# Kernel tuning notes

Hardware: AMD Instinct MI355X
Metric: run time of the kernel (lower is better)

The kernel has to match this reference:

```python
import jax, jax.numpy as jnp
import numpy as np

D = 512      # n_embd
H = 8        # n_head
L = 2        # n_layer (per stack)
T = 2048     # sequence length / block_size
B = 1        # batch
BANDS = (999, 9)  # band_width for [phase, tool] stacks
EPS = 1e-5


def _sinusoidal(n_pos, dim):
    pos = np.arange(n_pos)[:, None].astype(np.float64)
    j = np.arange(dim)[None, :]
    angle = pos / np.power(10000.0, 2 * (j // 2) / dim)
    out = np.zeros((n_pos, dim), np.float32)
    out[:, 0::2] = np.sin(angle[:, 0::2])
    out[:, 1::2] = np.cos(angle[:, 1::2])
    return jnp.asarray(out)


def setup_inputs() -> dict:
    key = jax.random.key(0)
    ks = jax.random.split(key, 8)
    s = 0.02
    rn = lambda k, shp: jax.random.normal(k, shp, jnp.float32) * s
    inp = {
        "x": jax.random.normal(ks[0], (B, T, D), jnp.float32),
        "pos_emb": _sinusoidal(T, D),            # sinusoidal, frozen
        # leading dim 2 = [phase stack, tool stack], then layer dim L
        "ln1_w": jnp.ones((2, L, D)), "ln1_b": jnp.zeros((2, L, D)),
        "ln2_w": jnp.ones((2, L, D)), "ln2_b": jnp.zeros((2, L, D)),
        "Wq": rn(ks[1], (2, L, D, D)), "bq": jnp.zeros((2, L, D)),
        "Wk": rn(ks[2], (2, L, D, D)), "bk": jnp.zeros((2, L, D)),
        "Wv": rn(ks[3], (2, L, D, D)), "bv": jnp.zeros((2, L, D)),
        "Wo": rn(ks[4], (2, L, D, D)), "bo": jnp.zeros((2, L, D)),
        "W1": rn(ks[5], (2, L, D, 2 * D)), "b1": jnp.zeros((2, L, 2 * D)),
        "W2": rn(ks[6], (2, L, 2 * D, D)), "b2": jnp.zeros((2, L, D)),
        "lnf_w": jnp.ones((D,)), "lnf_b": jnp.zeros((D,)),
    }
    return inp


def _ln(x, w, b):
    mu = x.mean(-1, keepdims=True)
    var = ((x - mu) ** 2).mean(-1, keepdims=True)
    return (x - mu) / jnp.sqrt(var + EPS) * w + b


def _attn(x, Wq, bq, Wk, bk, Wv, bv, Wo, bo, bw):
    Bx, Tx, _ = x.shape
    Dh = D // H
    heads = lambda W, b: (x @ W + b).reshape(Bx, Tx, H, Dh).transpose(0, 2, 1, 3)
    q, k, v = heads(Wq, bq), heads(Wk, bk), heads(Wv, bv)
    att = jnp.einsum('bhqd,bhkd->bhqk', q, k) / jnp.sqrt(jnp.float32(Dh))
    i = jnp.arange(Tx)[:, None]
    j = jnp.arange(Tx)[None, :]
    mask = (j <= i) & (j >= i - bw)  # causal band
    att = jnp.where(mask, att, -jnp.inf)
    att = jax.nn.softmax(att, axis=-1)
    y = jnp.einsum('bhqk,bhkd->bhqd', att, v).transpose(0, 2, 1, 3).reshape(Bx, Tx, D)
    return y @ Wo + bo


def reference(x, pos_emb, ln1_w, ln1_b, ln2_w, ln2_b,
              Wq, bq, Wk, bk, Wv, bv, Wo, bo,
              W1, b1, W2, b2, lnf_w, lnf_b):
    Tx = x.shape[1]
    h0 = x + pos_emb[None, :Tx]
    outs = []
    for s in range(2):  # phase stack, tool stack
        bw = BANDS[s]
        h = h0
        for l in range(L):
            h = h + _attn(_ln(h, ln1_w[s, l], ln1_b[s, l]),
                          Wq[s, l], bq[s, l], Wk[s, l], bk[s, l],
                          Wv[s, l], bv[s, l], Wo[s, l], bo[s, l], bw)
            hm = _ln(h, ln2_w[s, l], ln2_b[s, l])
            h = h + (jax.nn.gelu(hm @ W1[s, l] + b1[s, l], approximate=False)
                     @ W2[s, l] + b2[s, l])
        outs.append(_ln(h, lnf_w, lnf_b))
    return (outs[0], outs[1])
```

## Files before the change

### kernel.cpp

```cpp
#include <hip/hip_runtime.h>
#include <stdint.h>

#define T 2048
#define D 512
#define NH 8
#define DH 64
#define L 2

typedef float floatx4 __attribute__((ext_vector_type(4)));
typedef short shortx8 __attribute__((ext_vector_type(8)));
typedef unsigned short u16;
typedef unsigned short u16x4 __attribute__((ext_vector_type(4)));

__device__ __forceinline__ u16 f2bf(float f) {
    union { float f; uint32_t u; } c; c.f = f;
    uint32_t u = c.u;
    u += 0x7fffu + ((u >> 16) & 1u);
    return (u16)(u >> 16);
}

__device__ __forceinline__ float bf2f(u16 v) {
    union { uint32_t u; float f; } c; c.u = ((uint32_t)v) << 16;
    return c.f;
}

__device__ __forceinline__ void load_lds16(const void* g, void* l) {
    __builtin_amdgcn_global_load_lds((const __attribute__((address_space(1))) void*)g,
                                     (__attribute__((address_space(3))) void*)l,
                                     16, 0, 0);
}

struct TransJobs {
    const float* src[6];
    u16* dst[6];
    const float* x;
    const float* pos;
    u16* h;
};

__global__ __launch_bounds__(256) void pre_kernel(TransJobs j) {
    __shared__ float tile[32][33];
    int tid = threadIdx.x;
    if (blockIdx.z == 24) {
        int idx = (blockIdx.y * 32 + blockIdx.x) * 256 + tid;
        float4 xv = ((const float4*)j.x)[idx];
        float4 pv = ((const float4*)j.pos)[idx];
        u16x4 hh;
        hh[0] = f2bf(xv.x + pv.x); hh[1] = f2bf(xv.y + pv.y);
        hh[2] = f2bf(xv.z + pv.z); hh[3] = f2bf(xv.w + pv.w);
        ((u16x4*)j.h)[idx] = hh;
        ((u16x4*)j.h)[idx + (T * D / 4)] = hh;
        return;
    }
    int m = blockIdx.z >> 2, slice = blockIdx.z & 3;
    int R = (m == 5) ? 1024 : 512;
    int C = (m == 4) ? 1024 : 512;
    if (blockIdx.x * 32 >= C || blockIdx.y * 32 >= R) return;
    const float* in = j.src[m] + (size_t)slice * R * C;
    u16* out = j.dst[m] + (size_t)slice * R * C;
    int tx = tid & 31, ty = tid >> 5;
    int x = blockIdx.x * 32 + tx;
    int y0 = blockIdx.y * 32;
#pragma unroll
    for (int i = 0; i < 4; i++)
        tile[ty + i * 8][tx] = in[(size_t)(y0 + ty + i * 8) * C + x];
    __syncthreads();
    int ox = y0 + tx;
#pragma unroll
    for (int i = 0; i < 4; i++)
        out[(size_t)(blockIdx.x * 32 + ty + i * 8) * R + ox] = f2bf(tile[tx][ty + i * 8]);
}

__global__ __launch_bounds__(256) void ln_res_kernel(u16* __restrict__ h,
                                                     const u16* __restrict__ part,
                                                     const float* __restrict__ wp,
                                                     const float* __restrict__ bp,
                                                     u16* __restrict__ out, int l) {
    int row = blockIdx.x * 4 + (threadIdx.x >> 6);
    int lane = threadIdx.x & 63;
    int s = row >> 11;
    int c0 = lane * 4;
    u16* xr = h + (size_t)row * D;
    u16x4 h0 = *(const u16x4*)(xr + c0);
    u16x4 h1 = *(const u16x4*)(xr + c0 + 256);
    float4 v0, v1;
    v0.x = bf2f(h0[0]); v0.y = bf2f(h0[1]); v0.z = bf2f(h0[2]); v0.w = bf2f(h0[3]);
    v1.x = bf2f(h1[0]); v1.y = bf2f(h1[1]); v1.z = bf2f(h1[2]); v1.w = bf2f(h1[3]);
    if (part) {
        const u16* p0r = part + (size_t)s * 2 * T * D + (size_t)(row & (T - 1)) * D;
        const u16* p1r = p0r + (size_t)T * D;
        u16x4 a0 = *(const u16x4*)(p0r + c0), a1 = *(const u16x4*)(p0r + c0 + 256);
        u16x4 e0 = *(const u16x4*)(p1r + c0), e1 = *(const u16x4*)(p1r + c0 + 256);
        v0.x += bf2f(a0[0]) + bf2f(e0[0]); v0.y += bf2f(a0[1]) + bf2f(e0[1]);
        v0.z += bf2f(a0[2]) + bf2f(e0[2]); v0.w += bf2f(a0[3]) + bf2f(e0[3]);
        v1.x += bf2f(a1[0]) + bf2f(e1[0]); v1.y += bf2f(a1[1]) + bf2f(e1[1]);
        v1.z += bf2f(a1[2]) + bf2f(e1[2]); v1.w += bf2f(a1[3]) + bf2f(e1[3]);
        u16x4 s0, s1;
        s0[0] = f2bf(v0.x); s0[1] = f2bf(v0.y); s0[2] = f2bf(v0.z); s0[3] = f2bf(v0.w);
        s1[0] = f2bf(v1.x); s1[1] = f2bf(v1.y); s1[2] = f2bf(v1.z); s1[3] = f2bf(v1.w);
        *(u16x4*)(xr + c0) = s0;
        *(u16x4*)(xr + c0 + 256) = s1;
    }
    float sum = v0.x + v0.y + v0.z + v0.w + v1.x + v1.y + v1.z + v1.w;
    float sq = v0.x*v0.x + v0.y*v0.y + v0.z*v0.z + v0.w*v0.w
             + v1.x*v1.x + v1.y*v1.y + v1.z*v1.z + v1.w*v1.w;
#pragma unroll
    for (int d2 = 1; d2 < 64; d2 <<= 1) { sum += __shfl_xor(sum, d2); sq += __shfl_xor(sq, d2); }
    float mu = sum * (1.0f / D);
    float var = sq * (1.0f / D) - mu * mu;
    float rstd = rsqrtf(var + 1e-5f);
    const float* w = wp + (size_t)(s * L + l) * D;
    const float* b = bp + (size_t)(s * L + l) * D;
    u16x4 p0, p1;
#pragma unroll
    for (int jj = 0; jj < 4; jj++) {
        float a = (jj == 0 ? v0.x : jj == 1 ? v0.y : jj == 2 ? v0.z : v0.w);
        p0[jj] = f2bf((a - mu) * rstd * w[c0 + jj] + b[c0 + jj]);
        float c = (jj == 0 ? v1.x : jj == 1 ? v1.y : jj == 2 ? v1.z : v1.w);
        p1[jj] = f2bf((c - mu) * rstd * w[c0 + 256 + jj] + b[c0 + 256 + jj]);
    }
    *(u16x4*)(out + (size_t)row * D + c0) = p0;
    *(u16x4*)(out + (size_t)row * D + c0 + 256) = p1;
}

__global__ __launch_bounds__(256) void lnf_kernel(const u16* __restrict__ h,
                                                  const u16* __restrict__ part,
                                                  const float* __restrict__ w,
                                                  const float* __restrict__ b,
                                                  float* __restrict__ out) {
    int row = blockIdx.x * 4 + (threadIdx.x >> 6);
    int lane = threadIdx.x & 63;
    int s = row >> 11;
    int c0 = lane * 4;
    const u16* xr = h + (size_t)row * D;
    u16x4 h0 = *(const u16x4*)(xr + c0);
    u16x4 h1 = *(const u16x4*)(xr + c0 + 256);
    float4 v0, v1;
    v0.x = bf2f(h0[0]); v0.y = bf2f(h0[1]); v0.z = bf2f(h0[2]); v0.w = bf2f(h0[3]);
    v1.x = bf2f(h1[0]); v1.y = bf2f(h1[1]); v1.z = bf2f(h1[2]); v1.w = bf2f(h1[3]);
    const u16* p0r = part + (size_t)s * 2 * T * D + (size_t)(row & (T - 1)) * D;
    const u16* p1r = p0r + (size_t)T * D;
    u16x4 a0 = *(const u16x4*)(p0r + c0), a1 = *(const u16x4*)(p0r + c0 + 256);
    u16x4 e0 = *(const u16x4*)(p1r + c0), e1 = *(const u16x4*)(p1r + c0 + 256);
    v0.x += bf2f(a0[0]) + bf2f(e0[0]); v0.y += bf2f(a0[1]) + bf2f(e0[1]);
    v0.z += bf2f(a0[2]) + bf2f(e0[2]); v0.w += bf2f(a0[3]) + bf2f(e0[3]);
    v1.x += bf2f(a1[0]) + bf2f(e1[0]); v1.y += bf2f(a1[1]) + bf2f(e1[1]);
    v1.z += bf2f(a1[2]) + bf2f(e1[2]); v1.w += bf2f(a1[3]) + bf2f(e1[3]);
    float sum = v0.x + v0.y + v0.z + v0.w + v1.x + v1.y + v1.z + v1.w;
    float sq = v0.x*v0.x + v0.y*v0.y + v0.z*v0.z + v0.w*v0.w
             + v1.x*v1.x + v1.y*v1.y + v1.z*v1.z + v1.w*v1.w;
#pragma unroll
    for (int d2 = 1; d2 < 64; d2 <<= 1) { sum += __shfl_xor(sum, d2); sq += __shfl_xor(sq, d2); }
    float mu = sum * (1.0f / D);
    float var = sq * (1.0f / D) - mu * mu;
    float rstd = rsqrtf(var + 1e-5f);
    float4 r0, r1;
    r0.x = (v0.x - mu) * rstd * w[c0+0] + b[c0+0];
    r0.y = (v0.y - mu) * rstd * w[c0+1] + b[c0+1];
    r0.z = (v0.z - mu) * rstd * w[c0+2] + b[c0+2];
    r0.w = (v0.w - mu) * rstd * w[c0+3] + b[c0+3];
    r1.x = (v1.x - mu) * rstd * w[c0+256+0] + b[c0+256+0];
    r1.y = (v1.y - mu) * rstd * w[c0+256+1] + b[c0+256+1];
    r1.z = (v1.z - mu) * rstd * w[c0+256+2] + b[c0+256+2];
    r1.w = (v1.w - mu) * rstd * w[c0+256+3] + b[c0+256+3];
    *(float4*)(out + (size_t)row * D + c0) = r0;
    *(float4*)(out + (size_t)row * D + c0 + 256) = r1;
}

struct GemmPtrs {
    const u16* A[6];
    const u16* Bt[6];
    const float* bias[6];
    void* C[6];
};

#define EPI_QKV  0
#define EPI_GELU 1
#define EPI_PART 2

template <int EPI>
__global__ __launch_bounds__(256) void gemm_kernel(GemmPtrs p, int M, int N, int K, int KS) {
    __shared__ __align__(16) u16 smem[8192];
    u16* lA = smem;
    u16* lB = smem + 4096;
    int nchunk = K / KS;
    int pidx = blockIdx.z / nchunk;
    int kc = blockIdx.z % nchunk;
    int koff = kc * KS;
    const u16* A = p.A[pidx];
    const u16* Bt = p.Bt[pidx];
    int m0 = blockIdx.y * 64, n0 = blockIdx.x * 64;
    int tid = threadIdx.x;
    int lane = tid & 63, wave = tid >> 6;
    int wx = wave & 1, wy = wave >> 1;
    int l16 = lane & 15, q4 = lane >> 4;
    const u16* ag = A + (size_t)(m0 + (tid >> 2)) * K + koff + (tid & 3) * 8;
    const u16* bg = Bt + (size_t)(n0 + (tid >> 2)) * K + koff + (tid & 3) * 8;
    floatx4 acc[2][2] = {};
    for (int k0 = 0; k0 < KS; k0 += 64) {
        __syncthreads();
#pragma unroll
        for (int kh = 0; kh < 2; kh++) {
            load_lds16(ag + k0 + kh * 32, lA + kh * 2048 + tid * 8);
            load_lds16(bg + k0 + kh * 32, lB + kh * 2048 + tid * 8);
        }
        __syncthreads();
#pragma unroll
        for (int kh = 0; kh < 2; kh++) {
            shortx8 af[2], bf[2];
#pragma unroll
            for (int t = 0; t < 2; t++) {
                af[t] = *(const shortx8*)(lA + kh * 2048 + (wy * 32 + t * 16 + l16) * 32 + q4 * 8);
                bf[t] = *(const shortx8*)(lB + kh * 2048 + (wx * 32 + t * 16 + l16) * 32 + q4 * 8);
            }
#pragma unroll
            for (int i = 0; i < 2; i++)
#pragma unroll
                for (int j = 0; j < 2; j++)
                    acc[i][j] = __builtin_amdgcn_mfma_f32_16x16x32_bf16(af[i], bf[j], acc[i][j], 0, 0, 0);
        }
    }
    const float* bias = p.bias[pidx];
    __syncthreads();
    if (EPI == EPI_QKV && (pidx % 3 == 2)) {
#pragma unroll
        for (int i = 0; i < 2; i++) {
            int tl = wy * 32 + i * 16 + q4 * 4;
#pragma unroll
            for (int j = 0; j < 2; j++) {
                int dl = wx * 32 + j * 16 + l16;
                float bz = (kc == 0) ? bias[n0 + dl] : 0.0f;
                u16x4 pk;
#pragma unroll
                for (int r = 0; r < 4; r++) pk[r] = f2bf(acc[i][j][r] + bz);
                *(u16x4*)(smem + dl * 72 + tl) = pk;
            }
        }
        __syncthreads();
        int dl = tid >> 2, tc = (tid & 3) * 16;
        u16* dst = (u16*)p.C[pidx] + (size_t)(n0 + dl) * M + m0 + tc;
        shortx8 w0 = *(const shortx8*)(smem + dl * 72 + tc);
        shortx8 w1 = *(const shortx8*)(smem + dl * 72 + tc + 8);
        *(shortx8*)dst = w0;
        *(shortx8*)(dst + 8) = w1;
        return;
    }
#pragma unroll
    for (int i = 0; i < 2; i++) {
        int tl0 = wy * 32 + i * 16 + q4 * 4;
#pragma unroll
        for (int j = 0; j < 2; j++) {
            int dl = wx * 32 + j * 16 + l16;
            float bz = (kc == 0) ? bias[n0 + dl] : 0.0f;
#pragma unroll
            for (int r = 0; r < 4; r++) {
                float v = acc[i][j][r] + bz;
                if (EPI == EPI_GELU)
                    v = 0.5f * v * (1.0f + erff(v * 0.70710678118f));
                smem[(tl0 + r) * 72 + dl] = f2bf(v);
            }
        }
    }
    __syncthreads();
    {
        int tl = tid >> 2, dc = (tid & 3) * 16;
        u16* dst = (u16*)p.C[pidx]
                 + (EPI == EPI_PART ? (size_t)kc * M * N : (size_t)0)
                 + (size_t)(m0 + tl) * N + n0 + dc;
        shortx8 w0 = *(const shortx8*)(smem + tl * 72 + dc);
        shortx8 w1 = *(const shortx8*)(smem + tl * 72 + dc + 8);
        *(shortx8*)dst = w0;
        *(shortx8*)(dst + 8) = w1;
    }
}

__global__ __launch_bounds__(256) void attn_kernel(const u16* __restrict__ qg,
                                                   const u16* __restrict__ kg,
                                                   const u16* __restrict__ vtg,
                                                   u16* __restrict__ ao,
                                                   int bw0, int bw1) {
    __shared__ __align__(16) u16 pbuf[4][32 * 32];
    __shared__ float cl[2][32];
    __shared__ float co[2][32][64];
    int s = blockIdx.z, hh = blockIdx.y, q0 = blockIdx.x * 32;
    int bw = (s == 0) ? bw0 : bw1;
    int tid = threadIdx.x, wave = tid >> 6, lane = tid & 63;
    int l16 = lane & 15, q4 = lane >> 4;
    const u16* Q = qg + (size_t)s * T * D;
    const u16* Kp = kg + (size_t)s * T * D;
    const u16* V = vtg + (size_t)s * D * T;
    int hd = hh * DH;
    shortx8 qf[2][2];
#pragma unroll
    for (int g = 0; g < 2; g++)
#pragma unroll
        for (int hf = 0; hf < 2; hf++)
            qf[g][hf] = *(const shortx8*)(Q + (size_t)(q0 + g * 16 + l16) * D + hd + hf * 32 + q4 * 8);
    floatx4 o[2][4] = {};
    float lsum[2][4] = {};
    int klo = q0 - bw; if (klo < 0) klo = 0; klo &= ~31;
    int khi = q0 + 31;
    u16* pw = pbuf[wave];
    for (int kt = klo + wave * 32; kt <= khi; kt += 128) {
        shortx8 vf[4];
#pragma unroll
        for (int n = 0; n < 4; n++)
            vf[n] = *(const shortx8*)(V + (size_t)(hd + n * 16 + l16) * T + kt + q4 * 8);
        shortx8 kf[2][2];
#pragma unroll
        for (int t = 0; t < 2; t++)
#pragma unroll
            for (int hf = 0; hf < 2; hf++)
                kf[t][hf] = *(const shortx8*)(Kp + (size_t)(kt + t * 16 + l16) * D + hd + hf * 32 + q4 * 8);
        floatx4 sc[2][2] = {};
#pragma unroll
        for (int g = 0; g < 2; g++)
#pragma unroll
            for (int t = 0; t < 2; t++) {
                sc[g][t] = __builtin_amdgcn_mfma_f32_16x16x32_bf16(qf[g][0], kf[t][0], sc[g][t], 0, 0, 0);
                sc[g][t] = __builtin_amdgcn_mfma_f32_16x16x32_bf16(qf[g][1], kf[t][1], sc[g][t], 0, 0, 0);
            }
#pragma unroll
        for (int g = 0; g < 2; g++)
#pragma unroll
            for (int r = 0; r < 4; r++) {
                int row = q0 + g * 16 + q4 * 4 + r;
#pragma unroll
                for (int t = 0; t < 2; t++) {
                    int c = kt + t * 16 + l16;
                    float pv = (c <= row && c >= row - bw) ? __expf(sc[g][t][r] * 0.125f) : 0.0f;
                    lsum[g][r] += pv;
                    pw[(g * 16 + q4 * 4 + r) * 32 + t * 16 + l16] = f2bf(pv);
                }
            }
        shortx8 pf[2];
#pragma unroll
        for (int g = 0; g < 2; g++)
            pf[g] = *(const shortx8*)(pw + (g * 16 + l16) * 32 + q4 * 8);
#pragma unroll
        for (int g = 0; g < 2; g++)
#pragma unroll
            for (int n = 0; n < 4; n++)
                o[g][n] = __builtin_amdgcn_mfma_f32_16x16x32_bf16(pf[g], vf[n], o[g][n], 0, 0, 0);
    }
#pragma unroll
    for (int g = 0; g < 2; g++)
#pragma unroll
        for (int r = 0; r < 4; r++) {
#pragma unroll
            for (int d2 = 1; d2 < 16; d2 <<= 1) lsum[g][r] += __shfl_xor(lsum[g][r], d2);
        }
    if (wave >= 2) {
        if (l16 == 0) {
#pragma unroll
            for (int g = 0; g < 2; g++)
#pragma unroll
                for (int r = 0; r < 4; r++) cl[wave - 2][g * 16 + q4 * 4 + r] = lsum[g][r];
        }
#pragma unroll
        for (int g = 0; g < 2; g++)
#pragma unroll
            for (int n = 0; n < 4; n++)
#pragma unroll
                for (int r = 0; r < 4; r++)
                    co[wave - 2][g * 16 + q4 * 4 + r][n * 16 + l16] = o[g][n][r];
    }
    __syncthreads();
    if (wave < 2) {
        if (l16 == 0) {
#pragma unroll
            for (int g = 0; g < 2; g++)
#pragma unroll
                for (int r = 0; r < 4; r++) cl[wave][g * 16 + q4 * 4 + r] += lsum[g][r];
        }
#pragma unroll
        for (int g = 0; g < 2; g++)
#pragma unroll
            for (int n = 0; n < 4; n++)
#pragma unroll
                for (int r = 0; r < 4; r++)
                    co[wave][g * 16 + q4 * 4 + r][n * 16 + l16] += o[g][n][r];
    }
    __syncthreads();
#pragma unroll
    for (int i = 0; i < 8; i++) {
        int idx = tid + i * 256;
        int row = idx >> 6, col = idx & 63;
        float Ls = cl[0][row] + cl[1][row];
        float O = co[0][row][col] + co[1][row][col];
        ao[(size_t)s * T * D + (size_t)(q0 + row) * D + hd + col] = f2bf(O / Ls);
    }
}

extern "C" void kernel_launch(void* const* d_in, const int* in_sizes, int n_in,
                              void* d_out, int out_size, void* d_ws, size_t ws_size,
                              hipStream_t stream) {
    (void)in_sizes; (void)n_in; (void)out_size; (void)ws_size;
    const float* x     = (const float*)d_in[0];
    const float* pos   = (const float*)d_in[1];
    const float* ln1_w = (const float*)d_in[2];
    const float* ln1_b = (const float*)d_in[3];
    const float* ln2_w = (const float*)d_in[4];
    const float* ln2_b = (const float*)d_in[5];
    const float* Wq    = (const float*)d_in[6];
    const float* bq    = (const float*)d_in[7];
    const float* Wk    = (const float*)d_in[8];
    const float* bk    = (const float*)d_in[9];
    const float* Wv    = (const float*)d_in[10];
    const float* bv    = (const float*)d_in[11];
    const float* Wo    = (const float*)d_in[12];
    const float* bo    = (const float*)d_in[13];
    const float* W1    = (const float*)d_in[14];
    const float* b1    = (const float*)d_in[15];
    const float* W2    = (const float*)d_in[16];
    const float* b2    = (const float*)d_in[17];
    const float* lnf_w = (const float*)d_in[18];
    const float* lnf_b = (const float*)d_in[19];

    char* ws = (char*)d_ws;
    size_t off = 0;
    auto alloc = [&](size_t bytes) { void* p = ws + off; off += (bytes + 255) & ~(size_t)255; return p; };
    u16* WqT = (u16*)alloc((size_t)4 * 512 * 512 * 2);
    u16* WkT = (u16*)alloc((size_t)4 * 512 * 512 * 2);
    u16* WvT = (u16*)alloc((size_t)4 * 512 * 512 * 2);
    u16* WoT = (u16*)alloc((size_t)4 * 512 * 512 * 2);
    u16* W1T = (u16*)alloc((size_t)4 * 512 * 1024 * 2);
    u16* W2T = (u16*)alloc((size_t)4 * 1024 * 512 * 2);
    u16* h   = (u16*)alloc((size_t)2 * T * D * 2);
    u16* xln = (u16*)alloc((size_t)2 * T * D * 2);
    u16* qb  = (u16*)alloc((size_t)2 * T * D * 2);
    u16* kb  = (u16*)alloc((size_t)2 * T * D * 2);
    u16* vt  = (u16*)alloc((size_t)2 * T * D * 2);
    u16* ao  = (u16*)alloc((size_t)2 * T * D * 2);
    u16* ff  = (u16*)alloc((size_t)2 * T * 1024 * 2);
    u16* pp = (u16*)alloc((size_t)2 * 2 * T * D * 2);
    u16* pf = (u16*)alloc((size_t)2 * 2 * T * D * 2);

    TransJobs tj;
    tj.src[0] = Wq; tj.dst[0] = WqT;
    tj.src[1] = Wk; tj.dst[1] = WkT;
    tj.src[2] = Wv; tj.dst[2] = WvT;
    tj.src[3] = Wo; tj.dst[3] = WoT;
    tj.src[4] = W1; tj.dst[4] = W1T;
    tj.src[5] = W2; tj.dst[5] = W2T;
    tj.x = x; tj.pos = pos; tj.h = h;
    pre_kernel<<<dim3(32, 32, 25), 256, 0, stream>>>(tj);

    for (int l = 0; l < L; l++) {
        ln_res_kernel<<<(2 * T) / 4, 256, 0, stream>>>(h, l == 0 ? nullptr : pf,
                                                       ln1_w, ln1_b, xln, l);

        GemmPtrs g{};
        for (int s = 0; s < 2; s++) {
            int wo = s * L + l;
            const u16* a = xln + (size_t)s * T * D;
            g.A[s * 3 + 0] = a; g.Bt[s * 3 + 0] = WqT + (size_t)wo * 512 * 512;
            g.bias[s * 3 + 0] = bq + (size_t)wo * 512; g.C[s * 3 + 0] = qb + (size_t)s * T * D;
            g.A[s * 3 + 1] = a; g.Bt[s * 3 + 1] = WkT + (size_t)wo * 512 * 512;
            g.bias[s * 3 + 1] = bk + (size_t)wo * 512; g.C[s * 3 + 1] = kb + (size_t)s * T * D;
            g.A[s * 3 + 2] = a; g.Bt[s * 3 + 2] = WvT + (size_t)wo * 512 * 512;
            g.bias[s * 3 + 2] = bv + (size_t)wo * 512; g.C[s * 3 + 2] = vt + (size_t)s * T * D;
        }
        gemm_kernel<EPI_QKV><<<dim3(8, 32, 6), 256, 0, stream>>>(g, T, 512, 512, 512);

        attn_kernel<<<dim3(64, 8, 2), 256, 0, stream>>>(qb, kb, vt, ao, 999, 9);

        GemmPtrs gp{};
        for (int s = 0; s < 2; s++) {
            int wo = s * L + l;
            gp.A[s] = ao + (size_t)s * T * D;
            gp.Bt[s] = WoT + (size_t)wo * 512 * 512;
            gp.bias[s] = bo + (size_t)wo * 512;
            gp.C[s] = pp + (size_t)s * 2 * T * D;
        }
        gemm_kernel<EPI_PART><<<dim3(8, 32, 4), 256, 0, stream>>>(gp, T, 512, 512, 256);

        ln_res_kernel<<<(2 * T) / 4, 256, 0, stream>>>(h, pp, ln2_w, ln2_b, xln, l);

        GemmPtrs g1{};
        for (int s = 0; s < 2; s++) {
            int wo = s * L + l;
            g1.A[s] = xln + (size_t)s * T * D;
            g1.Bt[s] = W1T + (size_t)wo * 512 * 1024;
            g1.bias[s] = b1 + (size_t)wo * 1024;
            g1.C[s] = ff + (size_t)s * T * 1024;
        }
        gemm_kernel<EPI_GELU><<<dim3(16, 32, 2), 256, 0, stream>>>(g1, T, 1024, 512, 512);

        GemmPtrs g2{};
        for (int s = 0; s < 2; s++) {
            int wo = s * L + l;
            g2.A[s] = ff + (size_t)s * T * 1024;
            g2.Bt[s] = W2T + (size_t)wo * 1024 * 512;
            g2.bias[s] = b2 + (size_t)wo * 512;
            g2.C[s] = pf + (size_t)s * 2 * T * D;
        }
        gemm_kernel<EPI_PART><<<dim3(8, 32, 4), 256, 0, stream>>>(g2, T, 512, 1024, 512);
    }

    lnf_kernel<<<(2 * T) / 4, 256, 0, stream>>>(h, pf, lnf_w, lnf_b, (float*)d_out);
}
```

Baseline: 295.3 us.

## Split wide-band attention keys into chunks with a separate merge kernel

```diff
diff --git a/kernel.cpp b/kernel.cpp
--- a/kernel.cpp
+++ b/kernel.cpp
@@ -6,6 +6,8 @@
 #define NH 8
 #define DH 64
 #define L 2
+#define CHUNK 256
+#define NCHUNK 5
 
 typedef float floatx4 __attribute__((ext_vector_type(4)));
 typedef short shortx8 __attribute__((ext_vector_type(8)));
@@ -278,14 +280,29 @@
                                                    const u16* __restrict__ kg,
                                                    const u16* __restrict__ vtg,
                                                    u16* __restrict__ ao,
+                                                   float* __restrict__ po,
+                                                   float* __restrict__ pl,
                                                    int bw0, int bw1) {
     __shared__ __align__(16) u16 pbuf[4][32 * 32];
     __shared__ float cl[2][32];
     __shared__ float co[2][32][64];
-    int s = blockIdx.z, hh = blockIdx.y, q0 = blockIdx.x * 32;
-    int bw = (s == 0) ? bw0 : bw1;
+    int z = blockIdx.z;
+    int s = (z == NCHUNK) ? 1 : 0;
+    int chunk = s ? 0 : z;
+    int hh = blockIdx.y, q0 = blockIdx.x * 32;
+    int bw = s ? bw1 : bw0;
     int tid = threadIdx.x, wave = tid >> 6, lane = tid & 63;
     int l16 = lane & 15, q4 = lane >> 4;
+    int klo = q0 - bw; if (klo < 0) klo = 0; klo &= ~31;
+    int khi = q0 + 31;
+    int cstart, cend;
+    if (s == 0) {
+        cstart = klo + chunk * CHUNK;
+        if (cstart > khi) return;
+        cend = cstart + CHUNK - 1; if (cend > khi) cend = khi;
+    } else {
+        cstart = klo; cend = khi;
+    }
     const u16* Q = qg + (size_t)s * T * D;
     const u16* Kp = kg + (size_t)s * T * D;
     const u16* V = vtg + (size_t)s * D * T;
@@ -298,10 +315,8 @@
             qf[g][hf] = *(const shortx8*)(Q + (size_t)(q0 + g * 16 + l16) * D + hd + hf * 32 + q4 * 8);
     floatx4 o[2][4] = {};
     float lsum[2][4] = {};
-    int klo = q0 - bw; if (klo < 0) klo = 0; klo &= ~31;
-    int khi = q0 + 31;
     u16* pw = pbuf[wave];
-    for (int kt = klo + wave * 32; kt <= khi; kt += 128) {
+    for (int kt = cstart + wave * 32; kt <= cend; kt += 128) {
         shortx8 vf[4];
 #pragma unroll
         for (int n = 0; n < 4; n++)
@@ -382,14 +397,61 @@
                     co[wave][g * 16 + q4 * 4 + r][n * 16 + l16] += o[g][n][r];
     }
     __syncthreads();
-#pragma unroll
-    for (int i = 0; i < 8; i++) {
-        int idx = tid + i * 256;
-        int row = idx >> 6, col = idx & 63;
-        float Ls = cl[0][row] + cl[1][row];
-        float O = co[0][row][col] + co[1][row][col];
-        ao[(size_t)s * T * D + (size_t)(q0 + row) * D + hd + col] = f2bf(O / Ls);
-    }
+    if (s == 0) {
+        float* pob = po + ((size_t)chunk * T + q0) * D;
+#pragma unroll
+        for (int i = 0; i < 8; i++) {
+            int idx = tid + i * 256;
+            int row = idx >> 6, col = idx & 63;
+            float O = co[0][row][col] + co[1][row][col];
+            pob[(size_t)row * D + hd + col] = O;
+            if (col == 0) {
+                float Ls = cl[0][row] + cl[1][row];
+                pl[((size_t)chunk * T + q0 + row) * NH + hh] = Ls;
+            }
+        }
+    } else {
+#pragma unroll
+        for (int i = 0; i < 8; i++) {
+            int idx = tid + i * 256;
+            int row = idx >> 6, col = idx & 63;
+            float Ls = cl[0][row] + cl[1][row];
+            float O = co[0][row][col] + co[1][row][col];
+            ao[(size_t)s * T * D + (size_t)(q0 + row) * D + hd + col] = f2bf(O / Ls);
+        }
+    }
+}
+
+__global__ __launch_bounds__(256) void attn_merge_kernel(const float* __restrict__ po,
+                                                         const float* __restrict__ pl,
+                                                         u16* __restrict__ ao, int bw0) {
+    int row = blockIdx.x * 4 + (threadIdx.x >> 6);
+    int lane = threadIdx.x & 63;
+    int c0 = lane * 4;
+    int q0 = row & ~31;
+    int klo = q0 - bw0; if (klo < 0) klo = 0; klo &= ~31;
+    int cnt = (q0 + 31 - klo + CHUNK) / CHUNK;
+    int h0 = c0 >> 6, h1 = (c0 + 256) >> 6;
+    float a0x = 0, a0y = 0, a0z = 0, a0w = 0;
+    float a1x = 0, a1y = 0, a1z = 0, a1w = 0;
+    float l0 = 0, l1 = 0;
+    for (int c = 0; c < cnt; c++) {
+        const float* pr = po + ((size_t)c * T + row) * D;
+        float4 x0 = *(const float4*)(pr + c0);
+        float4 x1 = *(const float4*)(pr + c0 + 256);
+        a0x += x0.x; a0y += x0.y; a0z += x0.z; a0w += x0.w;
+        a1x += x1.x; a1y += x1.y; a1z += x1.z; a1w += x1.w;
+        const float* plr = pl + ((size_t)c * T + row) * NH;
+        l0 += plr[h0]; l1 += plr[h1];
+    }
+    float r0 = 1.0f / l0, r1 = 1.0f / l1;
+    u16x4 o0, o1;
+    o0[0] = f2bf(a0x * r0); o0[1] = f2bf(a0y * r0);
+    o0[2] = f2bf(a0z * r0); o0[3] = f2bf(a0w * r0);
+    o1[0] = f2bf(a1x * r1); o1[1] = f2bf(a1y * r1);
+    o1[2] = f2bf(a1z * r1); o1[3] = f2bf(a1w * r1);
+    *(u16x4*)(ao + (size_t)row * D + c0) = o0;
+    *(u16x4*)(ao + (size_t)row * D + c0 + 256) = o1;
 }
 
 extern "C" void kernel_launch(void* const* d_in, const int* in_sizes, int n_in,
@@ -435,6 +497,8 @@
     u16* ff  = (u16*)alloc((size_t)2 * T * 1024 * 2);
     u16* pp = (u16*)alloc((size_t)2 * 2 * T * D * 2);
     u16* pf = (u16*)alloc((size_t)2 * 2 * T * D * 2);
+    float* po = (float*)alloc((size_t)NCHUNK * T * D * 4);
+    float* pl = (float*)alloc((size_t)NCHUNK * T * NH * 4);
 
     TransJobs tj;
     tj.src[0] = Wq; tj.dst[0] = WqT;
@@ -463,7 +527,8 @@
         }
         gemm_kernel<EPI_QKV><<<dim3(8, 32, 6), 256, 0, stream>>>(g, T, 512, 512, 512);
 
-        attn_kernel<<<dim3(64, 8, 2), 256, 0, stream>>>(qb, kb, vt, ao, 999, 9);
+        attn_kernel<<<dim3(64, 8, NCHUNK + 1), 256, 0, stream>>>(qb, kb, vt, ao, po, pl, 999, 9);
+        attn_merge_kernel<<<T / 4, 256, 0, stream>>>(po, pl, ao, 999);
 
         GemmPtrs gp{};
         for (int s = 0; s < 2; s++) {
```

Result: slower. 319.5 us (+8.2%).
